# Kernel tuning notes

Hardware: AMD Instinct MI355X
Metric: run time of the kernel (lower is better)

The kernel has to match this reference:

```python
import jax, jax.numpy as jnp
import numpy as np

NUM_EMBEDDINGS = 1024
EMBEDDING_DIM = 64
COMMITMENT_COST = 0.25


def setup_inputs() -> dict:
    key = jax.random.key(0)
    k_in, k_w = jax.random.split(key)
    inputs = jax.random.normal(k_in, (32, 64, 32, 32), dtype=jnp.float32)
    # nn.Embedding weight initialized uniform(-1/K, 1/K)
    bound = 1.0 / NUM_EMBEDDINGS
    weight = jax.random.uniform(k_w, (NUM_EMBEDDINGS, EMBEDDING_DIM),
                                dtype=jnp.float32, minval=-bound, maxval=bound)
    return {"inputs": inputs, "weight": weight}


def reference(inputs, weight):
    # Flatten to [N, D] rows in embedding space
    flat = inputs.reshape(-1, EMBEDDING_DIM)  # [N, D]
    distances = (jnp.sum(flat * flat, axis=1, keepdims=True)
                 + jnp.sum(weight * weight, axis=1)
                 - 2.0 * jnp.matmul(flat, weight.T))
    encoding_indices = jnp.argmin(distances, axis=1)  # [N]
    quantized = weight[encoding_indices].reshape(inputs.shape)
    e_latent_loss = jnp.mean((jax.lax.stop_gradient(quantized) - inputs) ** 2)
    q_latent_loss = jnp.mean((quantized - jax.lax.stop_gradient(inputs)) ** 2)
    commitment_loss = COMMITMENT_COST * (q_latent_loss + e_latent_loss)
    # Straight-through estimator
    quantized = inputs + jax.lax.stop_gradient(quantized - inputs)
    return quantized, encoding_indices[:, None], commitment_loss
```

## Files before the change

### kernel.cpp

```cpp
#include <hip/hip_runtime.h>

#define NROWS  32768
#define DIM    64
#define KCODES 1024
#define NELEM  (NROWS * DIM)
#define CHUNKS 8
#define CPC    (KCODES / CHUNKS)

typedef float v2f __attribute__((ext_vector_type(2)));

__device__ __forceinline__ float np_sumsq64(const float v[64]) {
#pragma clang fp contract(off)
  float r0 = v[0] * v[0];
  float r1 = v[1] * v[1];
  float r2 = v[2] * v[2];
  float r3 = v[3] * v[3];
  float r4 = v[4] * v[4];
  float r5 = v[5] * v[5];
  float r6 = v[6] * v[6];
  float r7 = v[7] * v[7];
#pragma unroll
  for (int i = 8; i < 64; i += 8) {
    r0 += v[i + 0] * v[i + 0];
    r1 += v[i + 1] * v[i + 1];
    r2 += v[i + 2] * v[i + 2];
    r3 += v[i + 3] * v[i + 3];
    r4 += v[i + 4] * v[i + 4];
    r5 += v[i + 5] * v[i + 5];
    r6 += v[i + 6] * v[i + 6];
    r7 += v[i + 7] * v[i + 7];
  }
  return ((r0 + r1) + (r2 + r3)) + ((r4 + r5) + (r6 + r7));
}

__global__ __launch_bounds__(256) void vq_prep(const float* __restrict__ w,
                                               float* __restrict__ se,
                                               unsigned long long* __restrict__ keys) {
  const int t = blockIdx.x * 256 + threadIdx.x;
  keys[t] = ~0ull;

  if (t < KCODES) {
    float v[64];
    const float4* wr = (const float4*)(w + (size_t)t * DIM);
#pragma unroll
    for (int i = 0; i < 16; ++i) {
      float4 q = wr[i];
      v[4 * i + 0] = q.x; v[4 * i + 1] = q.y;
      v[4 * i + 2] = q.z; v[4 * i + 3] = q.w;
    }
    se[t] = np_sumsq64(v);
  }
}

__global__ __launch_bounds__(256)
__attribute__((amdgpu_waves_per_eu(4, 4)))
void vq_dist(const float* __restrict__ x,
             const float* __restrict__ w,
             const float* __restrict__ se,
             unsigned long long* __restrict__ keys) {
  const int bid = blockIdx.x;
  const int l = (bid & 7) * 128 + (bid >> 3);
  const int group = l >> 3;
  const int chunk = l & 7;
  const int t = threadIdx.x;
  const int row = group * 256 + t;
  const int c0 = chunk * CPC;

  v2f xv[32];
  const float4* xr = (const float4*)(x + (size_t)row * DIM);
#pragma unroll
  for (int i = 0; i < 16; ++i) {
    float4 q = xr[i];
    xv[2 * i + 0] = (v2f){q.x, q.y};
    xv[2 * i + 1] = (v2f){q.z, q.w};
  }
#pragma unroll
  for (int i = 0; i < 32; ++i) asm volatile("" : "+v"(xv[i]));

  float sx;
  {
#pragma clang fp contract(off)
    v2f A0 = xv[0] * xv[0], A1 = xv[1] * xv[1];
    v2f A2 = xv[2] * xv[2], A3 = xv[3] * xv[3];
#pragma unroll
    for (int m = 1; m < 8; ++m) {
      A0 += xv[4 * m + 0] * xv[4 * m + 0];
      A1 += xv[4 * m + 1] * xv[4 * m + 1];
      A2 += xv[4 * m + 2] * xv[4 * m + 2];
      A3 += xv[4 * m + 3] * xv[4 * m + 3];
    }
    sx = ((A0.x + A0.y) + (A1.x + A1.y)) + ((A2.x + A2.y) + (A3.x + A3.y));
  }

  const float4* w4 = (const float4*)w;
  float bd = __builtin_inff();
  int bc = 0;

#pragma unroll 2
  for (int j = 0; j < CPC; ++j) {
    const int c = c0 + j;
    const float4* wr = w4 + (size_t)c * 16;
    v2f a0 = (v2f){0.f, 0.f}, a1 = (v2f){0.f, 0.f};
    v2f a2 = (v2f){0.f, 0.f}, a3 = (v2f){0.f, 0.f};
#pragma unroll
    for (int i = 0; i < 16; i += 2) {
      float4 t0 = wr[i];
      float4 t1 = wr[i + 1];
      a0 += (v2f){t0.x, t0.y} * xv[2 * i + 0];
      a1 += (v2f){t0.z, t0.w} * xv[2 * i + 1];
      a2 += (v2f){t1.x, t1.y} * xv[2 * i + 2];
      a3 += (v2f){t1.z, t1.w} * xv[2 * i + 3];
    }
    v2f s01 = a0 + a1;
    v2f s23 = a2 + a3;
    v2f s = s01 + s23;
    float dot = s.x + s.y;
    float d = fmaf(-2.0f, dot, sx + se[c]);
    if (d < bd) { bd = d; bc = c; }
  }

  unsigned long long key =
      ((unsigned long long)__float_as_uint(bd) << 32) | (unsigned long long)(unsigned)bc;
  atomicMin(&keys[row], key);
}

__global__ __launch_bounds__(256) void vq_out(const float* __restrict__ x,
                                              const float* __restrict__ w,
                                              const unsigned long long* __restrict__ keys,
                                              float* __restrict__ outq,
                                              float* __restrict__ outidx,
                                              double* __restrict__ part) {
  __shared__ int sidx[32];
  __shared__ double sp[4];
  const int b = blockIdx.x, t = threadIdx.x;

  if (t < 32) {
    const int row = b * 32 + t;
    unsigned long long k = keys[row];
    const int idx = (int)(unsigned int)(k & 0xFFFFFFFFull);
    outidx[row] = (float)idx;
    sidx[t] = idx;
  }
  __syncthreads();

  double acc = 0.0;
  const float4* x4 = (const float4*)x;
  float4* o4 = (float4*)outq;
#pragma unroll
  for (int i = 0; i < 2; ++i) {
    const int e = i * 256 + t;
    const int rl = e >> 4;
    const int d4 = e & 15;
    const size_t gofs = ((size_t)b * 32 + rl) * 16 + d4;
    float4 xvv = x4[gofs];
    const float4* wr = (const float4*)(w + (size_t)sidx[rl] * DIM);
    float4 wv = wr[d4];
    float tx = wv.x - xvv.x, ty = wv.y - xvv.y;
    float tz = wv.z - xvv.z, tw = wv.w - xvv.w;
    float4 q;
    q.x = xvv.x + tx; q.y = xvv.y + ty;
    q.z = xvv.z + tz; q.w = xvv.w + tw;
    o4[gofs] = q;
    acc += (double)tx * tx + (double)ty * ty + (double)tz * tz + (double)tw * tw;
  }

#pragma unroll
  for (int s = 32; s > 0; s >>= 1) acc += __shfl_down(acc, s, 64);
  if ((t & 63) == 0) sp[t >> 6] = acc;
  __syncthreads();
  if (t == 0) part[b] = (sp[0] + sp[1]) + (sp[2] + sp[3]);
}

__global__ __launch_bounds__(256) void vq_fin(const double* __restrict__ part,
                                              float* __restrict__ outloss) {
  __shared__ double sp[4];
  const int t = threadIdx.x;
  double a = (part[t] + part[t + 256]) + (part[t + 512] + part[t + 768]);
#pragma unroll
  for (int s = 32; s > 0; s >>= 1) a += __shfl_down(a, s, 64);
  if ((t & 63) == 0) sp[t >> 6] = a;
  __syncthreads();
  if (t == 0) {
    double total = (sp[0] + sp[1]) + (sp[2] + sp[3]);
    *outloss = 0.5f * (float)(total / (double)NELEM);
  }
}

extern "C" void kernel_launch(void* const* d_in, const int* in_sizes, int n_in,
                              void* d_out, int out_size, void* d_ws, size_t ws_size,
                              hipStream_t stream) {
  const float* x = (const float*)d_in[0];
  const float* w = (const float*)d_in[1];

  float* outq    = (float*)d_out;
  float* outidx  = outq + NELEM;
  float* outloss = outidx + NROWS;

  char* wsb = (char*)d_ws;
  float* se    = (float*)(wsb + 256);
  double* part = (double*)(wsb + 8192);
  unsigned long long* keys = (unsigned long long*)(wsb + 147456);

  hipLaunchKernelGGL(vq_prep, dim3(128),  dim3(256), 0, stream, w, se, keys);
  hipLaunchKernelGGL(vq_dist, dim3(1024), dim3(256), 0, stream, x, w, se, keys);
  hipLaunchKernelGGL(vq_out,  dim3(1024), dim3(256), 0, stream, x, w, keys, outq, outidx, part);
  hipLaunchKernelGGL(vq_fin,  dim3(1),    dim3(256), 0, stream, part, outloss);
}
```

Before: 127.3 us.

## Register-block two rows per thread in VQ distance kernel and split codebook finer

```diff
diff --git a/kernel.cpp b/kernel.cpp
--- a/kernel.cpp
+++ b/kernel.cpp
@@ -4,8 +4,9 @@
 #define DIM    64
 #define KCODES 1024
 #define NELEM  (NROWS * DIM)
-#define CHUNKS 8
+#define CHUNKS 32
 #define CPC    (KCODES / CHUNKS)
+#define GROUPS 64
 
 typedef float v2f __attribute__((ext_vector_type(2)));
 
@@ -52,49 +53,61 @@
   }
 }
 
-__global__ __launch_bounds__(256)
-__attribute__((amdgpu_waves_per_eu(4, 4)))
+__global__ __launch_bounds__(256, 1)
 void vq_dist(const float* __restrict__ x,
              const float* __restrict__ w,
              const float* __restrict__ se,
              unsigned long long* __restrict__ keys) {
   const int bid = blockIdx.x;
-  const int l = (bid & 7) * 128 + (bid >> 3);
-  const int group = l >> 3;
-  const int chunk = l & 7;
+  const int xcd = bid & 7;
+  const int m = bid >> 3;
+  const int group = (xcd << 3) | (m >> 5);
+  const int chunk = m & 31;
   const int t = threadIdx.x;
-  const int row = group * 256 + t;
+  const int r0 = group * 512 + t;
+  const int r1 = r0 + 256;
   const int c0 = chunk * CPC;
-
-  v2f xv[32];
-  const float4* xr = (const float4*)(x + (size_t)row * DIM);
-#pragma unroll
-  for (int i = 0; i < 16; ++i) {
-    float4 q = xr[i];
-    xv[2 * i + 0] = (v2f){q.x, q.y};
-    xv[2 * i + 1] = (v2f){q.z, q.w};
-  }
-#pragma unroll
-  for (int i = 0; i < 32; ++i) asm volatile("" : "+v"(xv[i]));
-
-  float sx;
+  const float4* w4 = (const float4*)w;
+
+  v2f xa[32], xb[32];
+  {
+    const float4* xr0 = (const float4*)(x + (size_t)r0 * DIM);
+    const float4* xr1 = (const float4*)(x + (size_t)r1 * DIM);
+#pragma unroll
+    for (int i = 0; i < 16; ++i) {
+      float4 qa = xr0[i];
+      xa[2 * i + 0] = (v2f){qa.x, qa.y};
+      xa[2 * i + 1] = (v2f){qa.z, qa.w};
+      float4 qb = xr1[i];
+      xb[2 * i + 0] = (v2f){qb.x, qb.y};
+      xb[2 * i + 1] = (v2f){qb.z, qb.w};
+    }
+  }
+
+  float sxa, sxb;
   {
 #pragma clang fp contract(off)
-    v2f A0 = xv[0] * xv[0], A1 = xv[1] * xv[1];
-    v2f A2 = xv[2] * xv[2], A3 = xv[3] * xv[3];
-#pragma unroll
-    for (int m = 1; m < 8; ++m) {
-      A0 += xv[4 * m + 0] * xv[4 * m + 0];
-      A1 += xv[4 * m + 1] * xv[4 * m + 1];
-      A2 += xv[4 * m + 2] * xv[4 * m + 2];
-      A3 += xv[4 * m + 3] * xv[4 * m + 3];
-    }
-    sx = ((A0.x + A0.y) + (A1.x + A1.y)) + ((A2.x + A2.y) + (A3.x + A3.y));
-  }
-
-  const float4* w4 = (const float4*)w;
-  float bd = __builtin_inff();
-  int bc = 0;
+    v2f A0 = xa[0] * xa[0], A1 = xa[1] * xa[1];
+    v2f A2 = xa[2] * xa[2], A3 = xa[3] * xa[3];
+    v2f B0 = xb[0] * xb[0], B1 = xb[1] * xb[1];
+    v2f B2 = xb[2] * xb[2], B3 = xb[3] * xb[3];
+#pragma unroll
+    for (int mm = 1; mm < 8; ++mm) {
+      A0 += xa[4 * mm + 0] * xa[4 * mm + 0];
+      A1 += xa[4 * mm + 1] * xa[4 * mm + 1];
+      A2 += xa[4 * mm + 2] * xa[4 * mm + 2];
+      A3 += xa[4 * mm + 3] * xa[4 * mm + 3];
+      B0 += xb[4 * mm + 0] * xb[4 * mm + 0];
+      B1 += xb[4 * mm + 1] * xb[4 * mm + 1];
+      B2 += xb[4 * mm + 2] * xb[4 * mm + 2];
+      B3 += xb[4 * mm + 3] * xb[4 * mm + 3];
+    }
+    sxa = ((A0.x + A0.y) + (A1.x + A1.y)) + ((A2.x + A2.y) + (A3.x + A3.y));
+    sxb = ((B0.x + B0.y) + (B1.x + B1.y)) + ((B2.x + B2.y) + (B3.x + B3.y));
+  }
+
+  float bda = __builtin_inff(); int bca = 0;
+  float bdb = __builtin_inff(); int bcb = 0;
 
 #pragma unroll 2
   for (int j = 0; j < CPC; ++j) {
@@ -102,26 +115,43 @@
     const float4* wr = w4 + (size_t)c * 16;
     v2f a0 = (v2f){0.f, 0.f}, a1 = (v2f){0.f, 0.f};
     v2f a2 = (v2f){0.f, 0.f}, a3 = (v2f){0.f, 0.f};
+    v2f b0 = (v2f){0.f, 0.f}, b1 = (v2f){0.f, 0.f};
+    v2f b2 = (v2f){0.f, 0.f}, b3 = (v2f){0.f, 0.f};
 #pragma unroll
     for (int i = 0; i < 16; i += 2) {
       float4 t0 = wr[i];
       float4 t1 = wr[i + 1];
-      a0 += (v2f){t0.x, t0.y} * xv[2 * i + 0];
-      a1 += (v2f){t0.z, t0.w} * xv[2 * i + 1];
-      a2 += (v2f){t1.x, t1.y} * xv[2 * i + 2];
-      a3 += (v2f){t1.z, t1.w} * xv[2 * i + 3];
-    }
-    v2f s01 = a0 + a1;
-    v2f s23 = a2 + a3;
-    v2f s = s01 + s23;
-    float dot = s.x + s.y;
-    float d = fmaf(-2.0f, dot, sx + se[c]);
-    if (d < bd) { bd = d; bc = c; }
-  }
-
-  unsigned long long key =
-      ((unsigned long long)__float_as_uint(bd) << 32) | (unsigned long long)(unsigned)bc;
-  atomicMin(&keys[row], key);
+      a0 += (v2f){t0.x, t0.y} * xa[2 * i + 0];
+      a1 += (v2f){t0.z, t0.w} * xa[2 * i + 1];
+      a2 += (v2f){t1.x, t1.y} * xa[2 * i + 2];
+      a3 += (v2f){t1.z, t1.w} * xa[2 * i + 3];
+      b0 += (v2f){t0.x, t0.y} * xb[2 * i + 0];
+      b1 += (v2f){t0.z, t0.w} * xb[2 * i + 1];
+      b2 += (v2f){t1.x, t1.y} * xb[2 * i + 2];
+      b3 += (v2f){t1.z, t1.w} * xb[2 * i + 3];
+    }
+    {
+      v2f s01 = a0 + a1;
+      v2f s23 = a2 + a3;
+      v2f s = s01 + s23;
+      float dot = s.x + s.y;
+      float d = fmaf(-2.0f, dot, sxa + se[c]);
+      if (d < bda) { bda = d; bca = c; }
+    }
+    {
+      v2f s01 = b0 + b1;
+      v2f s23 = b2 + b3;
+      v2f s = s01 + s23;
+      float dot = s.x + s.y;
+      float d = fmaf(-2.0f, dot, sxb + se[c]);
+      if (d < bdb) { bdb = d; bcb = c; }
+    }
+  }
+
+  atomicMin(&keys[r0], ((unsigned long long)__float_as_uint(bda) << 32) |
+                           (unsigned long long)(unsigned)bca);
+  atomicMin(&keys[r1], ((unsigned long long)__float_as_uint(bdb) << 32) |
+                           (unsigned long long)(unsigned)bcb);
 }
 
 __global__ __launch_bounds__(256) void vq_out(const float* __restrict__ x,
@@ -202,7 +232,7 @@
   unsigned long long* keys = (unsigned long long*)(wsb + 147456);
 
   hipLaunchKernelGGL(vq_prep, dim3(128),  dim3(256), 0, stream, w, se, keys);
-  hipLaunchKernelGGL(vq_dist, dim3(1024), dim3(256), 0, stream, x, w, se, keys);
+  hipLaunchKernelGGL(vq_dist, dim3(2048), dim3(256), 0, stream, x, w, se, keys);
   hipLaunchKernelGGL(vq_out,  dim3(1024), dim3(256), 0, stream, x, w, keys, outq, outidx, part);
   hipLaunchKernelGGL(vq_fin,  dim3(1),    dim3(256), 0, stream, part, outloss);
 }
```

Result: slower. 130.0 us (+2.1%).

## Fuse VQ prep, distance, output and loss into one kernel with last-block epilogues

Applied to the files above, without the earlier changes.

```diff
diff --git a/kernel.cpp b/kernel.cpp
--- a/kernel.cpp
+++ b/kernel.cpp
@@ -6,6 +6,8 @@
 #define NELEM  (NROWS * DIM)
 #define CHUNKS 8
 #define CPC    (KCODES / CHUNKS)
+#define GROUPS 128
+#define GRID   (GROUPS * CHUNKS)
 
 typedef float v2f __attribute__((ext_vector_type(2)));
 
@@ -33,31 +35,20 @@
   return ((r0 + r1) + (r2 + r3)) + ((r4 + r5) + (r6 + r7));
 }
 
-__global__ __launch_bounds__(256) void vq_prep(const float* __restrict__ w,
-                                               float* __restrict__ se,
-                                               unsigned long long* __restrict__ keys) {
-  const int t = blockIdx.x * 256 + threadIdx.x;
-  keys[t] = ~0ull;
-
-  if (t < KCODES) {
-    float v[64];
-    const float4* wr = (const float4*)(w + (size_t)t * DIM);
-#pragma unroll
-    for (int i = 0; i < 16; ++i) {
-      float4 q = wr[i];
-      v[4 * i + 0] = q.x; v[4 * i + 1] = q.y;
-      v[4 * i + 2] = q.z; v[4 * i + 3] = q.w;
-    }
-    se[t] = np_sumsq64(v);
-  }
-}
-
-__global__ __launch_bounds__(256)
-__attribute__((amdgpu_waves_per_eu(4, 4)))
-void vq_dist(const float* __restrict__ x,
-             const float* __restrict__ w,
-             const float* __restrict__ se,
-             unsigned long long* __restrict__ keys) {
+__global__ __launch_bounds__(256, 4)
+void vq_fused(const float* __restrict__ x,
+              const float* __restrict__ w,
+              unsigned long long* __restrict__ keys,
+              unsigned int* __restrict__ gcnt,
+              unsigned int* __restrict__ fincnt,
+              double* __restrict__ part,
+              float* __restrict__ outq,
+              float* __restrict__ outidx,
+              float* __restrict__ outloss) {
+  __shared__ float se_lds[CPC];
+  __shared__ double sp[4];
+  __shared__ int sflag, finflag;
+
   const int bid = blockIdx.x;
   const int l = (bid & 7) * 128 + (bid >> 3);
   const int group = l >> 3;
@@ -66,6 +57,18 @@
   const int row = group * 256 + t;
   const int c0 = chunk * CPC;
 
+  if (t < CPC) {
+    float v[64];
+    const float4* wr = (const float4*)(w + (size_t)(c0 + t) * DIM);
+#pragma unroll
+    for (int i = 0; i < 16; ++i) {
+      float4 q = wr[i];
+      v[4 * i + 0] = q.x; v[4 * i + 1] = q.y;
+      v[4 * i + 2] = q.z; v[4 * i + 3] = q.w;
+    }
+    se_lds[t] = np_sumsq64(v);
+  }
+
   v2f xv[32];
   const float4* xr = (const float4*)(x + (size_t)row * DIM);
 #pragma unroll
@@ -91,6 +94,8 @@
     }
     sx = ((A0.x + A0.y) + (A1.x + A1.y)) + ((A2.x + A2.y) + (A3.x + A3.y));
   }
+
+  __syncthreads();
 
   const float4* w4 = (const float4*)w;
   float bd = __builtin_inff();
@@ -115,69 +120,62 @@
     v2f s23 = a2 + a3;
     v2f s = s01 + s23;
     float dot = s.x + s.y;
-    float d = fmaf(-2.0f, dot, sx + se[c]);
+    float d = fmaf(-2.0f, dot, sx + se_lds[j]);
     if (d < bd) { bd = d; bc = c; }
   }
 
-  unsigned long long key =
-      ((unsigned long long)__float_as_uint(bd) << 32) | (unsigned long long)(unsigned)bc;
-  atomicMin(&keys[row], key);
-}
-
-__global__ __launch_bounds__(256) void vq_out(const float* __restrict__ x,
-                                              const float* __restrict__ w,
-                                              const unsigned long long* __restrict__ keys,
-                                              float* __restrict__ outq,
-                                              float* __restrict__ outidx,
-                                              double* __restrict__ part) {
-  __shared__ int sidx[32];
-  __shared__ double sp[4];
-  const int b = blockIdx.x, t = threadIdx.x;
-
-  if (t < 32) {
-    const int row = b * 32 + t;
-    unsigned long long k = keys[row];
-    const int idx = (int)(unsigned int)(k & 0xFFFFFFFFull);
-    outidx[row] = (float)idx;
-    sidx[t] = idx;
-  }
-  __syncthreads();
+  atomicMin(&keys[row], ((unsigned long long)__float_as_uint(bd) << 32) |
+                            (unsigned long long)(unsigned)bc);
+
+  __threadfence();
+  if (t == 0) {
+    unsigned int old = atomicAdd(&gcnt[group], 1u);
+    sflag = (old == (unsigned int)(CHUNKS - 2)) ? 1 : 0;
+  }
+  __syncthreads();
+  if (!sflag) return;
+  __threadfence();
+
+  unsigned long long k = atomicMin(&keys[row], ~0ull);
+  const int idx = (int)(unsigned int)(k & 0xFFFFFFFFull);
+  outidx[row] = (float)idx;
 
   double acc = 0.0;
-  const float4* x4 = (const float4*)x;
-  float4* o4 = (float4*)outq;
-#pragma unroll
-  for (int i = 0; i < 2; ++i) {
-    const int e = i * 256 + t;
-    const int rl = e >> 4;
-    const int d4 = e & 15;
-    const size_t gofs = ((size_t)b * 32 + rl) * 16 + d4;
-    float4 xvv = x4[gofs];
-    const float4* wr = (const float4*)(w + (size_t)sidx[rl] * DIM);
-    float4 wv = wr[d4];
-    float tx = wv.x - xvv.x, ty = wv.y - xvv.y;
-    float tz = wv.z - xvv.z, tw = wv.w - xvv.w;
-    float4 q;
-    q.x = xvv.x + tx; q.y = xvv.y + ty;
-    q.z = xvv.z + tz; q.w = xvv.w + tw;
-    o4[gofs] = q;
-    acc += (double)tx * tx + (double)ty * ty + (double)tz * tz + (double)tw * tw;
+  {
+    const float4* wr = (const float4*)(w + (size_t)idx * DIM);
+    float4* oq = (float4*)(outq + (size_t)row * DIM);
+#pragma unroll
+    for (int i = 0; i < 16; ++i) {
+      float4 wv = wr[i];
+      const v2f xlo = xv[2 * i], xhi = xv[2 * i + 1];
+      float tx = wv.x - xlo.x, ty = wv.y - xlo.y;
+      float tz = wv.z - xhi.x, tw = wv.w - xhi.y;
+      float4 q;
+      q.x = xlo.x + tx; q.y = xlo.y + ty;
+      q.z = xhi.x + tz; q.w = xhi.y + tw;
+      oq[i] = q;
+      acc += (double)tx * tx + (double)ty * ty + (double)tz * tz + (double)tw * tw;
+    }
   }
 
 #pragma unroll
   for (int s = 32; s > 0; s >>= 1) acc += __shfl_down(acc, s, 64);
   if ((t & 63) == 0) sp[t >> 6] = acc;
   __syncthreads();
-  if (t == 0) part[b] = (sp[0] + sp[1]) + (sp[2] + sp[3]);
-}
-
-__global__ __launch_bounds__(256) void vq_fin(const double* __restrict__ part,
-                                              float* __restrict__ outloss) {
-  __shared__ double sp[4];
-  const int t = threadIdx.x;
-  double a = (part[t] + part[t + 256]) + (part[t + 512] + part[t + 768]);
+  if (t == 0) {
+    part[group] = (sp[0] + sp[1]) + (sp[2] + sp[3]);
+    __threadfence();
+    unsigned int old = atomicAdd(fincnt, 1u);
+    finflag = (old == (unsigned int)(GROUPS - 2)) ? 1 : 0;
+  }
+  __syncthreads();
+  if (!finflag) return;
+  __threadfence();
+
+  double a = (t < GROUPS) ? atomicAdd(&part[t], 0.0) : 0.0;
 #pragma unroll
   for (int s = 32; s > 0; s >>= 1) a += __shfl_down(a, s, 64);
+  __syncthreads();
   if ((t & 63) == 0) sp[t >> 6] = a;
   __syncthreads();
   if (t == 0) {
@@ -197,12 +195,12 @@
   float* outloss = outidx + NROWS;
 
   char* wsb = (char*)d_ws;
-  float* se    = (float*)(wsb + 256);
-  double* part = (double*)(wsb + 8192);
-  unsigned long long* keys = (unsigned long long*)(wsb + 147456);
-
-  hipLaunchKernelGGL(vq_prep, dim3(128),  dim3(256), 0, stream, w, se, keys);
-  hipLaunchKernelGGL(vq_dist, dim3(1024), dim3(256), 0, stream, x, w, se, keys);
-  hipLaunchKernelGGL(vq_out,  dim3(1024), dim3(256), 0, stream, x, w, keys, outq, outidx, part);
-  hipLaunchKernelGGL(vq_fin,  dim3(1),    dim3(256), 0, stream, part, outloss);
+  unsigned long long* keys = (unsigned long long*)wsb;
+  unsigned int* gcnt   = (unsigned int*)(wsb + 262144);
+  unsigned int* fincnt = (unsigned int*)(wsb + 262144 + 512);
+  double* part = (double*)(wsb + 263168);
+
+  hipMemsetAsync(wsb, 0xFF, 262144 + 512 + 64, stream);
+  hipLaunchKernelGGL(vq_fused, dim3(GRID), dim3(256), 0, stream,
+                     x, w, keys, gcnt, fincnt, part, outq, outidx, outloss);
 }
```

After: 215.9 us. 1.7x slower.
